# Performance work log

Hardware: AMD Instinct MI355X
Metric: run time of the kernel (lower is better)

Reference implementation:

```python
import jax, jax.numpy as jnp
import numpy as np

B, S, DIM, COV = 64, 512, 1024, 256


def setup_inputs() -> dict:
    key = jax.random.key(0)
    ks = jax.random.split(key, 12)
    s = 0.02
    h = jax.random.normal(ks[0], (B, DIM), jnp.float32)
    context = jax.random.normal(ks[1], (B, S, DIM), jnp.float32)
    cov = jax.random.normal(ks[2], (B, S, COV), jnp.float32)
    mask = jax.random.randint(ks[3], (B, S), 0, 2) == 1
    W_in = jax.random.normal(ks[4], (DIM, DIM), jnp.float32) * s
    W_out = jax.random.normal(ks[5], (DIM, 2 * DIM), jnp.float32) * s
    W_cov = jax.random.normal(ks[6], (DIM, COV), jnp.float32) * s
    b_cov = jax.random.normal(ks[7], (DIM,), jnp.float32) * s
    w_ih = jax.random.normal(ks[8], (3 * COV, 2 * DIM + 1), jnp.float32) * s
    w_hh = jax.random.normal(ks[9], (3 * COV, COV), jnp.float32) * s
    b_ih = jax.random.normal(ks[10], (3 * COV,), jnp.float32) * s
    b_hh = jax.random.normal(ks[11], (3 * COV,), jnp.float32) * s
    return dict(h=h, context=context, cov=cov, W_in=W_in, W_out=W_out,
                W_cov=W_cov, b_cov=b_cov, w_ih=w_ih, w_hh=w_hh,
                b_ih=b_ih, b_hh=b_hh, mask=mask)


def reference(h, context, cov, W_in, W_out, W_cov, b_cov, w_ih, w_hh, b_ih, b_hh, mask):
    # coverage-adjusted context: context + cov_linear(cov)  [B,S,DIM]
    ctx = context + jnp.einsum('bsc,dc->bsd', cov, W_cov) + b_cov
    # target = linear_in(h)  [B,DIM]
    target = h @ W_in.T
    # scores = bmm(context, target).squeeze(2)  [B,S]
    attn = jnp.einsum('bsd,bd->bs', ctx, target)
    attn = jnp.where(mask, -jnp.inf, attn)
    attn = jax.nn.softmax(attn, axis=1)
    # weighted_context = bmm(attn3, context)  [B,DIM]
    wc = jnp.einsum('bs,bsd->bd', attn, ctx)
    h_tilde = jnp.tanh(jnp.concatenate([wc, h], axis=1) @ W_out.T)
    # single-step GRU coverage update over B*S rows
    h_exp = jnp.broadcast_to(h[:, None, :], (B, S, DIM))
    x = jnp.concatenate([ctx, h_exp, attn[..., None]], axis=-1).reshape(B * S, 2 * DIM + 1)
    h0 = cov.reshape(B * S, COV)
    gx = x @ w_ih.T + b_ih   # [B*S, 3*COV]
    gh = h0 @ w_hh.T + b_hh  # [B*S, 3*COV]
    xr, xz, xn = jnp.split(gx, 3, axis=1)
    hr, hz, hn = jnp.split(gh, 3, axis=1)
    r = jax.nn.sigmoid(xr + hr)
    z = jax.nn.sigmoid(xz + hz)
    n = jnp.tanh(xn + r * hn)
    new_cov = ((1.0 - z) * n + z * h0).reshape(B, S, COV)
    return h_tilde, attn, new_cov
```

## Files before the change

kernel.cpp:

```cpp
#include <hip/hip_runtime.h>
#include <math.h>

typedef unsigned short ushort_t;
typedef __attribute__((ext_vector_type(8))) short short8;
typedef __attribute__((ext_vector_type(4))) float f32x4;
typedef __attribute__((ext_vector_type(4))) unsigned short ushort4v;

constexpr int B_ = 64, S_ = 512, DIM_ = 1024, COV_ = 256, TC_ = 768, KIH_ = 2049;
constexpr int NG_ = 1024, KG_ = 1280;

__device__ __forceinline__ float b2f(ushort_t u) {
    union { unsigned int i; float f; } v; v.i = ((unsigned int)u) << 16; return v.f;
}
__device__ __forceinline__ ushort_t f2b(float f) {
    unsigned int x = __float_as_uint(f);
    unsigned int r = x + 0x7fffu + ((x >> 16) & 1u);
    return (ushort_t)(r >> 16);
}
__device__ __forceinline__ float ldv(const float* p, size_t i) { return p[i]; }
__device__ __forceinline__ float ldv(const ushort_t* p, size_t i) { return b2f(p[i]); }

__device__ __forceinline__ float wave_reduce(float a) {
#pragma unroll
    for (int off = 32; off >= 1; off >>= 1) a += __shfl_down(a, off, 64);
    return a;
}

__device__ __forceinline__ void xpose4(f32x4& v, int l) {
    float s, r;
    s = (l & 1) ? v[0] : v[1]; r = __shfl_xor(s, 1, 64); if (l & 1) v[0] = r; else v[1] = r;
    s = (l & 1) ? v[2] : v[3]; r = __shfl_xor(s, 1, 64); if (l & 1) v[2] = r; else v[3] = r;
    s = (l & 2) ? v[0] : v[2]; r = __shfl_xor(s, 2, 64); if (l & 2) v[0] = r; else v[2] = r;
    s = (l & 2) ? v[1] : v[3]; r = __shfl_xor(s, 2, 64); if (l & 2) v[1] = r; else v[3] = r;
}

#define GLDS16(src, dst)                                                            \
    __builtin_amdgcn_global_load_lds(                                               \
        (const __attribute__((address_space(1))) void*)(src),                       \
        (__attribute__((address_space(3))) void*)(dst), 16, 0, 0)

__global__ void k_detect(const unsigned char* __restrict__ mask,
                         const ushort_t* __restrict__ win,
                         int* __restrict__ flags) {
    __shared__ int red0[256];
    __shared__ int red1[256];
    int tid = threadIdx.x, mb = 0, f32 = 0;
    for (int i = tid; i < 32768; i += 256)
        if ((i & 3) != 0 && mask[i] != 0) mb = 1;
    for (int i = tid; i < 32768; i += 256) {
        ushort_t u = win[2 * i];
        if ((u & 0x7F80u) >= 0x4480u) f32 = 1;
    }
    red0[tid] = mb; red1[tid] = f32; __syncthreads();
    for (int st = 128; st >= 1; st >>= 1) {
        if (tid < st) { red0[tid] |= red0[tid + st]; red1[tid] |= red1[tid + st]; }
        __syncthreads();
    }
    if (tid == 0) { flags[0] = red0[0]; flags[1] = red1[0]; }
}

template <typename IT>
__device__ __forceinline__ void transpose_body(const IT* __restrict__ in,
                                               ushort_t* __restrict__ out,
                                               int R, int C, int ld, int off) {
    int idx = blockIdx.x * 256 + threadIdx.x;
    if (idx >= R * C) return;
    int r = idx / C, c = idx - r * C;
    out[c * R + r] = f2b(ldv(in, (size_t)r * ld + off + c));
}
__global__ void k_transpose(const void* __restrict__ in, ushort_t* __restrict__ out,
                            int R, int C, int ld, int off, const int* __restrict__ flags) {
    if (flags[1]) transpose_body((const float*)in, out, R, C, ld, off);
    else transpose_body((const ushort_t*)in, out, R, C, ld, off);
}

template <typename IT>
__device__ __forceinline__ void watt_body(const IT* __restrict__ wih, float* __restrict__ watt) {
    int j = threadIdx.x;
    watt[j] = ldv(wih, (size_t)j * KIH_ + 2048);
}
__global__ void k_watt(const void* __restrict__ wih, float* __restrict__ watt,
                       const int* __restrict__ flags) {
    if (flags[1]) watt_body((const float*)wih, watt);
    else watt_body((const ushort_t*)wih, watt);
}

template <typename IT>
__device__ __forceinline__ void bfold_body(const IT* __restrict__ bcov,
                                           const IT* __restrict__ wih,
                                           float* __restrict__ bfold) {
    int j = blockIdx.x * 4 + (threadIdx.x >> 6);
    int lane = threadIdx.x & 63;
    const IT* wr = wih + (size_t)j * KIH_;
    float a = 0.f;
#pragma unroll
    for (int i = 0; i < 16; ++i) { int k = lane + 64 * i; a += ldv(bcov, k) * ldv(wr, k); }
    a = wave_reduce(a);
    if (lane == 0) bfold[j] = a;
}
__global__ __launch_bounds__(256) void k_bfold(const void* __restrict__ bcov,
                                               const void* __restrict__ wih,
                                               float* __restrict__ bfold,
                                               const int* __restrict__ flags) {
    if (flags[1]) bfold_body((const float*)bcov, (const float*)wih, bfold);
    else bfold_body((const ushort_t*)bcov, (const ushort_t*)wih, bfold);
}

__global__ __launch_bounds__(256) void k_wfold(const ushort_t* __restrict__ wcov_t,
                                               const ushort_t* __restrict__ w_t,
                                               float* __restrict__ wfold) {
    __shared__ float col[DIM_];
    int c = blockIdx.x, tid = threadIdx.x;
    for (int d = tid; d < DIM_; d += 256) col[d] = b2f(wcov_t[c * DIM_ + d]);
    __syncthreads();
    float a0 = 0.f, a1 = 0.f, a2 = 0.f;
    for (int d = 0; d < DIM_; ++d) {
        float x = col[d];
        const ushort_t* wr = w_t + d * TC_;
        a0 += x * b2f(wr[tid]);
        a1 += x * b2f(wr[tid + 256]);
        a2 += x * b2f(wr[tid + 512]);
    }
    wfold[c * TC_ + tid] = a0;
    wfold[c * TC_ + tid + 256] = a1;
    wfold[c * TC_ + tid + 512] = a2;
}

template <typename IT>
__device__ __forceinline__ void buildwg_body(const IT* __restrict__ wih,
                                             const IT* __restrict__ whh,
                                             const float* __restrict__ wfold,
                                             ushort_t* __restrict__ wg) {
    int idx = blockIdx.x * 256 + threadIdx.x;
    if (idx >= NG_ * KG_) return;
    int n = idx / KG_, k = idx - n * KG_;
    int g = n & 3, cq = n >> 2;
    int j = g * COV_ + cq;
    float v;
    if (k < DIM_) {
        v = (j < TC_) ? ldv(wih, (size_t)j * KIH_ + k) : 0.f;
    } else {
        int c = k - DIM_;
        if (j < 512)      v = wfold[c * TC_ + j] + ldv(whh, (size_t)j * COV_ + c);
        else if (j < TC_) v = wfold[c * TC_ + j];
        else              v = ldv(whh, (size_t)(j - 256) * COV_ + c);
    }
    wg[(size_t)n * KG_ + k] = f2b(v);
}
__global__ void k_buildwg(const void* __restrict__ wih, const void* __restrict__ whh,
                          const float* __restrict__ wfold, ushort_t* __restrict__ wg,
                          const int* __restrict__ flags) {
    if (flags[1]) buildwg_body((const float*)wih, (const float*)whh, wfold, wg);
    else buildwg_body((const ushort_t*)wih, (const ushort_t*)whh, wfold, wg);
}

template <typename IT>
__device__ __forceinline__ void target_body(const IT* __restrict__ h,
                                            const IT* __restrict__ W_in,
                                            float* __restrict__ target) {
    int o = blockIdx.x * 4 + (threadIdx.x >> 6);
    int lane = threadIdx.x & 63;
    int b = o >> 10, d = o & (DIM_ - 1);
    const IT* hr = h + (size_t)b * DIM_;
    const IT* wr = W_in + (size_t)d * DIM_;
    float a = 0.f;
#pragma unroll
    for (int j = 0; j < 16; ++j) { int k = lane + 64 * j; a += ldv(hr, k) * ldv(wr, k); }
    a = wave_reduce(a);
    if (lane == 0) target[o] = a;
}
__global__ __launch_bounds__(256) void k_target_w(const void* __restrict__ h,
                                                  const void* __restrict__ W_in,
                                                  float* __restrict__ target,
                                                  const int* __restrict__ flags) {
    if (flags[1]) target_body((const float*)h, (const float*)W_in, target);
    else target_body((const ushort_t*)h, (const ushort_t*)W_in, target);
}

template <typename IT>
__device__ __forceinline__ void mvec_body(const float* __restrict__ target,
                                          const IT* __restrict__ W_cov,
                                          const IT* __restrict__ bcov,
                                          float* __restrict__ mvec,
                                          float* __restrict__ bct) {
    __shared__ float tg[DIM_];
    __shared__ float red[256];
    int b = blockIdx.x, tid = threadIdx.x;
    float pb = 0.f;
    for (int k = tid; k < DIM_; k += 256) {
        float t = target[b * DIM_ + k];
        tg[k] = t; pb += t * ldv(bcov, k);
    }
    red[tid] = pb; __syncthreads();
    for (int st = 128; st >= 1; st >>= 1) {
        if (tid < st) red[tid] += red[tid + st];
        __syncthreads();
    }
    float acc = 0.f;
    for (int d = 0; d < DIM_; ++d) acc += tg[d] * ldv(W_cov, (size_t)d * COV_ + tid);
    mvec[b * COV_ + tid] = acc;
    if (tid == 0) bct[b] = red[0];
}
__global__ __launch_bounds__(256) void k_mvec(const float* __restrict__ target,
                                              const void* __restrict__ W_cov,
                                              const void* __restrict__ bcov,
                                              float* __restrict__ mvec,
                                              float* __restrict__ bct,
                                              const int* __restrict__ flags) {
    if (flags[1]) mvec_body(target, (const float*)W_cov, (const float*)bcov, mvec, bct);
    else mvec_body(target, (const ushort_t*)W_cov, (const ushort_t*)bcov, mvec, bct);
}

template <typename IT>
__device__ __forceinline__ void scoreraw_body(const IT* __restrict__ context,
                                              const IT* __restrict__ cov,
                                              const float* __restrict__ target,
                                              const float* __restrict__ mvec,
                                              const float* __restrict__ bct,
                                              float* __restrict__ scf,
                                              ushort_t* __restrict__ ctx_bf,
                                              ushort_t* __restrict__ cov_bf) {
    __shared__ float tg[DIM_];
    __shared__ float ms[COV_];
    int b = blockIdx.x, tid = threadIdx.x;
    for (int k = tid; k < DIM_; k += 256) tg[k] = target[b * DIM_ + k];
    if (tid < COV_) ms[tid] = mvec[b * COV_ + tid];
    float bc = bct[b];
    __syncthreads();
    int wave = tid >> 6, lane = tid & 63;
    int s0 = blockIdx.y * 64 + wave * 16;
    for (int i = 0; i < 16; ++i) {
        int s = s0 + i;
        size_t row = (size_t)(b * S_ + s);
        const IT* cr = context + row * DIM_;
        const IT* vr = cov + row * COV_;
        float a = 0.f;
        if constexpr (sizeof(IT) == 4) {
#pragma unroll
            for (int j = 0; j < 4; ++j) {
                int d = lane * 4 + 256 * j;
                float4 x = *(const float4*)((const float*)cr + d);
                a += x.x * tg[d] + x.y * tg[d + 1] + x.z * tg[d + 2] + x.w * tg[d + 3];
                if (ctx_bf) {
                    ushort4v u;
                    u[0] = f2b(x.x); u[1] = f2b(x.y); u[2] = f2b(x.z); u[3] = f2b(x.w);
                    *(ushort4v*)(ctx_bf + row * DIM_ + d) = u;
                }
            }
            {
                int cc = lane * 4;
                float4 x = *(const float4*)((const float*)vr + cc);
                a += x.x * ms[cc] + x.y * ms[cc + 1] + x.z * ms[cc + 2] + x.w * ms[cc + 3];
                if (cov_bf) {
                    ushort4v u;
                    u[0] = f2b(x.x); u[1] = f2b(x.y); u[2] = f2b(x.z); u[3] = f2b(x.w);
                    *(ushort4v*)(cov_bf + row * COV_ + cc) = u;
                }
            }
        } else {
#pragma unroll
            for (int j = 0; j < 16; ++j) { int d = lane + 64 * j; a += ldv(cr, d) * tg[d]; }
#pragma unroll
            for (int j = 0; j < 4; ++j) { int c = lane + 64 * j; a += ldv(vr, c) * ms[c]; }
        }
        a = wave_reduce(a);
        if (lane == 0) scf[row] = a + bc;
    }
}
__global__ __launch_bounds__(256) void k_scoreraw(const void* __restrict__ context,
                                                  const void* __restrict__ cov,
                                                  const float* __restrict__ target,
                                                  const float* __restrict__ mvec,
                                                  const float* __restrict__ bct,
                                                  float* __restrict__ scf,
                                                  ushort_t* __restrict__ ctx_bf,
                                                  ushort_t* __restrict__ cov_bf,
                                                  const int* __restrict__ flags) {
    if (flags[1]) scoreraw_body((const float*)context, (const float*)cov, target, mvec, bct,
                                scf, ctx_bf, cov_bf);
    else scoreraw_body((const ushort_t*)context, (const ushort_t*)cov, target, mvec, bct,
                       scf, ctx_bf, cov_bf);
}

__global__ __launch_bounds__(256) void k_softmax(const float* __restrict__ scf,
                                                 const void* __restrict__ maskp,
                                                 const int* __restrict__ flags,
                                                 float* __restrict__ attnf,
                                                 float* __restrict__ attn_out) {
    __shared__ float red[256];
    int b = blockIdx.x, tid = threadIdx.x;
    int mb = flags[0];
    int i0 = b * S_ + tid, i1 = i0 + 256;
    int m0 = mb ? (int)((const unsigned char*)maskp)[i0] : ((const int*)maskp)[i0];
    int m1 = mb ? (int)((const unsigned char*)maskp)[i1] : ((const int*)maskp)[i1];
    float s0 = m0 ? -INFINITY : scf[i0];
    float s1 = m1 ? -INFINITY : scf[i1];
    red[tid] = fmaxf(s0, s1); __syncthreads();
    for (int st = 128; st >= 1; st >>= 1) {
        if (tid < st) red[tid] = fmaxf(red[tid], red[tid + st]);
        __syncthreads();
    }
    float mx = red[0]; __syncthreads();
    float e0 = expf(s0 - mx), e1 = expf(s1 - mx);
    red[tid] = e0 + e1; __syncthreads();
    for (int st = 128; st >= 1; st >>= 1) {
        if (tid < st) red[tid] += red[tid + st];
        __syncthreads();
    }
    float inv = 1.0f / red[0];
    float a0 = e0 * inv, a1 = e1 * inv;
    attnf[i0] = a0; attnf[i1] = a1;
    attn_out[i0] = a0; attn_out[i1] = a1;
}

__global__ __launch_bounds__(256) void k_wcpart2(const ushort_t* __restrict__ ctx_bf,
                                                 const ushort_t* __restrict__ cov_bf,
                                                 const void* __restrict__ ctx_in,
                                                 const void* __restrict__ cov_in,
                                                 const float* __restrict__ attnf,
                                                 float* __restrict__ wc8,
                                                 float* __restrict__ ac8,
                                                 const int* __restrict__ flags) {
    const ushort_t* C = flags[1] ? ctx_bf : (const ushort_t*)ctx_in;
    const ushort_t* V = flags[1] ? cov_bf : (const ushort_t*)cov_in;
    __shared__ float at[64];
    int b = blockIdx.x, ch = blockIdx.y, tid = threadIdx.x;
    int s0 = ch * 64;
    if (tid < 64) at[tid] = attnf[b * S_ + s0 + tid];
    __syncthreads();
    float acv = 0.f;
    for (int s = 0; s < 64; ++s)
        acv += at[s] * b2f(V[((size_t)(b * S_ + s0 + s)) * COV_ + tid]);
    ac8[((size_t)ch * B_ + b) * COV_ + tid] = acv;
    float acc[4] = {0.f, 0.f, 0.f, 0.f};
    for (int s = 0; s < 64; ++s) {
        float w = at[s];
        const ushort_t* cr = C + ((size_t)(b * S_ + s0 + s)) * DIM_;
        acc[0] += w * b2f(cr[tid]);
        acc[1] += w * b2f(cr[tid + 256]);
        acc[2] += w * b2f(cr[tid + 512]);
        acc[3] += w * b2f(cr[tid + 768]);
    }
    size_t base = ((size_t)ch * B_ + b) * DIM_;
    for (int m = 0; m < 4; ++m) wc8[base + tid + 256 * m] = acc[m];
}

template <typename IT>
__device__ __forceinline__ void wcfin_body(const float* __restrict__ wc8,
                                           const float* __restrict__ ac8,
                                           const ushort_t* __restrict__ wcov_t,
                                           const IT* __restrict__ bcov,
                                           float* __restrict__ wc) {
    __shared__ float ac[COV_];
    int b = blockIdx.x, tid = threadIdx.x;
    float a = 0.f;
    for (int ch = 0; ch < 8; ++ch) a += ac8[((size_t)ch * B_ + b) * COV_ + tid];
    ac[tid] = a;
    __syncthreads();
    float acc[4] = {0.f, 0.f, 0.f, 0.f};
    for (int ch = 0; ch < 8; ++ch) {
        size_t base = ((size_t)ch * B_ + b) * DIM_;
        for (int m = 0; m < 4; ++m) acc[m] += wc8[base + tid + 256 * m];
    }
    for (int c = 0; c < COV_; ++c) {
        float av = ac[c];
        const ushort_t* wr = wcov_t + c * DIM_;
        acc[0] += av * b2f(wr[tid]);
        acc[1] += av * b2f(wr[tid + 256]);
        acc[2] += av * b2f(wr[tid + 512]);
        acc[3] += av * b2f(wr[tid + 768]);
    }
    for (int m = 0; m < 4; ++m) {
        int d = tid + 256 * m;
        wc[b * DIM_ + d] = acc[m] + ldv(bcov, d);
    }
}
__global__ __launch_bounds__(256) void k_wcfin(const float* __restrict__ wc8,
                                               const float* __restrict__ ac8,
                                               const ushort_t* __restrict__ wcov_t,
                                               const void* __restrict__ bcov,
                                               float* __restrict__ wc,
                                               const int* __restrict__ flags) {
    if (flags[1]) wcfin_body(wc8, ac8, wcov_t, (const float*)bcov, wc);
    else wcfin_body(wc8, ac8, wcov_t, (const ushort_t*)bcov, wc);
}

template <typename IT>
__device__ __forceinline__ void htilde_body(const float* __restrict__ wc,
                                            const IT* __restrict__ h,
                                            const IT* __restrict__ W_out,
                                            float* __restrict__ out_ht) {
    int o = blockIdx.x * 4 + (threadIdx.x >> 6);
    int lane = threadIdx.x & 63;
    int b = o >> 10, d = o & (DIM_ - 1);
    const float* wcr = wc + b * DIM_;
    const IT* hr = h + (size_t)b * DIM_;
    const IT* wr = W_out + (size_t)d * 2 * DIM_;
    float a = 0.f;
#pragma unroll
    for (int j = 0; j < 16; ++j) { int k = lane + 64 * j; a += wcr[k] * ldv(wr, k); }
#pragma unroll
    for (int j = 0; j < 16; ++j) { int k = lane + 64 * j; a += ldv(hr, k) * ldv(wr, DIM_ + k); }
    a = wave_reduce(a);
    if (lane == 0) out_ht[o] = tanhf(a);
}
__global__ __launch_bounds__(256) void k_htilde_w(const float* __restrict__ wc,
                                                  const void* __restrict__ h,
                                                  const void* __restrict__ W_out,
                                                  float* __restrict__ out_ht,
                                                  const int* __restrict__ flags) {
    if (flags[1]) htilde_body(wc, (const float*)h, (const float*)W_out, out_ht);
    else htilde_body(wc, (const ushort_t*)h, (const ushort_t*)W_out, out_ht);
}

template <typename IT>
__device__ __forceinline__ void gxh_body(const IT* __restrict__ h,
                                         const IT* __restrict__ w_ih,
                                         const IT* __restrict__ b_ih,
                                         const float* __restrict__ bfold,
                                         float* __restrict__ gxall) {
    int o = blockIdx.x * 4 + (threadIdx.x >> 6);
    int lane = threadIdx.x & 63;
    int b = o / TC_, j = o - b * TC_;
    const IT* hr = h + (size_t)b * DIM_;
    const IT* wr = w_ih + (size_t)j * KIH_ + DIM_;
    float a = 0.f;
#pragma unroll
    for (int i = 0; i < 16; ++i) { int k = lane + 64 * i; a += ldv(hr, k) * ldv(wr, k); }
    a = wave_reduce(a);
    if (lane == 0) gxall[o] = a + ldv(b_ih, j) + bfold[j];
}
__global__ __launch_bounds__(256) void k_gxh_w(const void* __restrict__ h,
                                               const void* __restrict__ w_ih,
                                               const void* __restrict__ b_ih,
                                               const float* __restrict__ bfold,
                                               float* __restrict__ gxall,
                                               const int* __restrict__ flags) {
    if (flags[1]) gxh_body((const float*)h, (const float*)w_ih, (const float*)b_ih, bfold, gxall);
    else gxh_body((const ushort_t*)h, (const ushort_t*)w_ih, (const ushort_t*)b_ih, bfold, gxall);
}

__global__ __launch_bounds__(256) void k_gemm5(const ushort_t* __restrict__ ctx_bf,
                                               const ushort_t* __restrict__ cov_bf,
                                               const void* __restrict__ ctx_in,
                                               const void* __restrict__ cov_in,
                                               const ushort_t* __restrict__ wg,
                                               const float* __restrict__ attnf,
                                               const float* __restrict__ gxall,
                                               const float* __restrict__ watt,
                                               const void* __restrict__ bhh,
                                               float* __restrict__ out_cov,
                                               const int* __restrict__ flags) {
    const int f32in = flags[1];
    const ushort_t* Xc = f32in ? ctx_bf : (const ushort_t*)ctx_in;
    const ushort_t* Xv = f32in ? cov_bf : (const ushort_t*)cov_in;
    __shared__ __align__(16) unsigned char smem[2 * 128 * 33 * 4];
    ushort_t* A0 = (ushort_t*)smem;
    ushort_t* B0 = A0 + 128 * 32;
    ushort_t* A1 = B0 + 128 * 32;
    ushort_t* B1 = A1 + 128 * 32;
    float* smN = (float*)smem;
    float* smZ = smN + 128 * 33;

    int tid = threadIdx.x;
    int p = blockIdx.x;
    int xcd = p & 7, t = p >> 3;
    int nb = t & 7, rb = xcd + 8 * (t >> 3);
    int n0 = nb * 128;
    int grow0 = rb * 128;
    int wave = tid >> 6, lane = tid & 63;
    int wm = wave >> 1, wn = wave & 1;
    int half = lane >> 4, r16 = lane & 15;

    int c0 = wave * 128 + lane;
    int ra0 = c0 >> 2, sa0 = (c0 & 3) ^ ((ra0 >> 1) & 3);
    int c1 = c0 + 64;
    int ra1 = c1 >> 2, sa1 = (c1 & 3) ^ ((ra1 >> 1) & 3);

    const ushort_t* gA0c = Xc + (size_t)(grow0 + ra0) * DIM_ + sa0 * 8;
    const ushort_t* gA1c = Xc + (size_t)(grow0 + ra1) * DIM_ + sa1 * 8;
    const ushort_t* gA0v = Xv + (size_t)(grow0 + ra0) * COV_ + sa0 * 8;
    const ushort_t* gA1v = Xv + (size_t)(grow0 + ra1) * COV_ + sa1 * 8;
    const ushort_t* gB0p = wg + (size_t)(n0 + ra0) * KG_ + sa0 * 8;
    const ushort_t* gB1p = wg + (size_t)(n0 + ra1) * KG_ + sa1 * 8;
    int ldsd0 = wave * 1024;
    int ldsd1 = wave * 1024 + 512;

    int offA[4], offB[4];
#pragma unroll
    for (int u = 0; u < 4; ++u) {
        int rA = wm * 64 + u * 16 + r16;
        offA[u] = rA * 32 + (half ^ ((rA >> 1) & 3)) * 8;
        int rB = wn * 64 + u * 16 + r16;
        offB[u] = rB * 32 + (half ^ ((rB >> 1) & 3)) * 8;
    }

    f32x4 acc[4][4];
#pragma unroll
    for (int i = 0; i < 4; ++i)
#pragma unroll
        for (int j = 0; j < 4; ++j) acc[i][j] = (f32x4){0.f, 0.f, 0.f, 0.f};

    auto stage = [&](int kt, ushort_t* Ad, ushort_t* Bd) {
        int k0 = kt * 32;
        const ushort_t *pa0, *pa1;
        if (k0 < DIM_) { pa0 = gA0c + k0; pa1 = gA1c + k0; }
        else           { int kk = k0 - DIM_; pa0 = gA0v + kk; pa1 = gA1v + kk; }
        GLDS16(pa0, Ad + ldsd0);
        GLDS16(pa1, Ad + ldsd1);
        GLDS16(gB0p + k0, Bd + ldsd0);
        GLDS16(gB1p + k0, Bd + ldsd1);
    };
    auto compute = [&](const ushort_t* Ac, const ushort_t* Bc) {
        short8 a[4], b[4];
#pragma unroll
        for (int u = 0; u < 4; ++u) a[u] = *(const short8*)&Ac[offA[u]];
#pragma unroll
        for (int u = 0; u < 4; ++u) b[u] = *(const short8*)&Bc[offB[u]];
#pragma unroll
        for (int i = 0; i < 4; ++i)
#pragma unroll
            for (int j = 0; j < 4; ++j)
                acc[i][j] = __builtin_amdgcn_mfma_f32_16x16x32_bf16(a[i], b[j], acc[i][j], 0, 0, 0);
    };

    constexpr int NT = KG_ / 32;
    stage(0, A0, B0);
    __syncthreads();
#pragma unroll 1
    for (int kt = 0; kt < NT; kt += 2) {
        stage(kt + 1, A1, B1);
        compute(A0, B0);
        __syncthreads();
        if (kt + 2 < NT) stage(kt + 2, A0, B0);
        compute(A1, B1);
        __syncthreads();
    }

    int l = lane;
    int bb = grow0 >> 9;
    const float* gx = gxall + bb * TC_;
    int rloc[4]; float atv[4];
#pragma unroll
    for (int i = 0; i < 4; ++i) {
        rloc[i] = wm * 64 + 16 * i + ((l >> 4) << 2) + (l & 3);
        atv[i] = attnf[grow0 + rloc[i]];
    }
#pragma unroll
    for (int j = 0; j < 4; ++j) {
        int cl = wn * 16 + 4 * j + ((l >> 2) & 3);
        int c = (n0 >> 2) + cl;
        float gxR = gx[c], gxZ = gx[COV_ + c], gxN = gx[2 * COV_ + c];
        float waR = watt[c], waZ = watt[COV_ + c], waN = watt[2 * COV_ + c];
        float bhR, bhZ, bhN;
        if (f32in) {
            const float* bp = (const float*)bhh;
            bhR = bp[c]; bhZ = bp[COV_ + c]; bhN = bp[2 * COV_ + c];
        } else {
            const ushort_t* bp = (const ushort_t*)bhh;
            bhR = b2f(bp[c]); bhZ = b2f(bp[COV_ + c]); bhN = b2f(bp[2 * COV_ + c]);
        }
#pragma unroll
        for (int i = 0; i < 4; ++i) {
            f32x4 v = acc[i][j];
            xpose4(v, l);
            float at = atv[i];
            float aR  = v[0] + gxR + at * waR + bhR;
            float aZ  = v[1] + gxZ + at * waZ + bhZ;
            float aXN = v[2] + gxN + at * waN;
            float aHN = v[3] + bhN;
            float r = 1.f / (1.f + expf(-aR));
            float z = 1.f / (1.f + expf(-aZ));
            float nn = tanhf(aXN + r * aHN);
            smN[rloc[i] * 33 + cl] = nn;
            smZ[rloc[i] * 33 + cl] = z;
        }
    }
    __syncthreads();
    int cbase = nb * 32;
    for (int u = tid; u < 128 * 8; u += 256) {
        int rl = u >> 3, c4 = (u & 7) * 4;
        float n0v = smN[rl * 33 + c4 + 0], n1v = smN[rl * 33 + c4 + 1];
        float n2v = smN[rl * 33 + c4 + 2], n3v = smN[rl * 33 + c4 + 3];
        float z0 = smZ[rl * 33 + c4 + 0], z1 = smZ[rl * 33 + c4 + 1];
        float z2 = smZ[rl * 33 + c4 + 2], z3 = smZ[rl * 33 + c4 + 3];
        size_t base = (size_t)(grow0 + rl) * COV_ + cbase + c4;
        float h0v, h1v, h2v, h3v;
        if (f32in) {
            float4 hv = *(const float4*)((const float*)cov_in + base);
            h0v = hv.x; h1v = hv.y; h2v = hv.z; h3v = hv.w;
        } else {
            ushort4v hv = *(const ushort4v*)((const ushort_t*)cov_in + base);
            h0v = b2f(hv[0]); h1v = b2f(hv[1]); h2v = b2f(hv[2]); h3v = b2f(hv[3]);
        }
        float4 o;
        o.x = (1.f - z0) * n0v + z0 * h0v;
        o.y = (1.f - z1) * n1v + z1 * h1v;
        o.z = (1.f - z2) * n2v + z2 * h2v;
        o.w = (1.f - z3) * n3v + z3 * h3v;
        *(float4*)(out_cov + base) = o;
    }
}

template <typename IT>
__device__ __forceinline__ void gru_body(const IT* __restrict__ context,
                                         const IT* __restrict__ cov,
                                         const float* __restrict__ attnf,
                                         const float* __restrict__ gxall,
                                         const float* __restrict__ watt,
                                         const ushort_t* __restrict__ w_t,
                                         const float* __restrict__ wfold,
                                         const ushort_t* __restrict__ whh_t,
                                         const IT* __restrict__ bhh,
                                         float* __restrict__ out_cov) {
    __shared__ float xc[8][DIM_];
    __shared__ float h0s[8][COV_];
    __shared__ float atn[8];
    int base = blockIdx.x * 8, tid = threadIdx.x;
    int b = base / S_;
    for (int i = tid; i < 8 * DIM_; i += 256)
        ((float*)xc)[i] = ldv(context, (size_t)base * DIM_ + i);
    for (int i = tid; i < 8 * COV_; i += 256)
        ((float*)h0s)[i] = ldv(cov, (size_t)base * COV_ + i);
    if (tid < 8) atn[tid] = attnf[base + tid];
    __syncthreads();
    int c = tid;
    float gxR = gxall[b * TC_ + c], gxZ = gxall[b * TC_ + 256 + c], gxN = gxall[b * TC_ + 512 + c];
    float bhR = ldv(bhh, c), bhZ = ldv(bhh, 256 + c), bhN = ldv(bhh, 512 + c);
    float waR = watt[c], waZ = watt[256 + c], waN = watt[512 + c];
    float aR[8], aZ[8], aXN[8], aHN[8];
#pragma unroll
    for (int g = 0; g < 8; ++g) {
        float a = atn[g];
        aR[g] = gxR + bhR + a * waR;
        aZ[g] = gxZ + bhZ + a * waZ;
        aXN[g] = gxN + a * waN;
        aHN[g] = bhN;
    }
    for (int k = 0; k < DIM_; ++k) {
        const ushort_t* row = w_t + k * TC_;
        float wr = b2f(row[c]), wz = b2f(row[256 + c]), wn = b2f(row[512 + c]);
#pragma unroll
        for (int g = 0; g < 8; ++g) {
            float x = xc[g][k];
            aR[g] += x * wr; aZ[g] += x * wz; aXN[g] += x * wn;
        }
    }
    for (int k = 0; k < COV_; ++k) {
        const float* row = wfold + k * TC_;
        float wr = row[c], wz = row[256 + c], wn = row[512 + c];
#pragma unroll
        for (int g = 0; g < 8; ++g) {
            float x = h0s[g][k];
            aR[g] += x * wr; aZ[g] += x * wz; aXN[g] += x * wn;
        }
    }
    for (int k = 0; k < COV_; ++k) {
        const ushort_t* row = whh_t + k * TC_;
        float wr = b2f(row[c]), wz = b2f(row[256 + c]), wn = b2f(row[512 + c]);
#pragma unroll
        for (int g = 0; g < 8; ++g) {
            float hh = h0s[g][k];
            aR[g] += hh * wr; aZ[g] += hh * wz; aHN[g] += hh * wn;
        }
    }
#pragma unroll
    for (int g = 0; g < 8; ++g) {
        float r = 1.f / (1.f + expf(-aR[g]));
        float z = 1.f / (1.f + expf(-aZ[g]));
        float n = tanhf(aXN[g] + r * aHN[g]);
        float h0c = h0s[g][c];
        out_cov[(size_t)(base + g) * COV_ + c] = (1.f - z) * n + z * h0c;
    }
}
__global__ __launch_bounds__(256) void k_gru_f(const void* __restrict__ context,
                                               const void* __restrict__ cov,
                                               const float* __restrict__ attnf,
                                               const float* __restrict__ gxall,
                                               const float* __restrict__ watt,
                                               const ushort_t* __restrict__ w_t,
                                               const float* __restrict__ wfold,
                                               const ushort_t* __restrict__ whh_t,
                                               const void* __restrict__ bhh,
                                               float* __restrict__ out_cov,
                                               const int* __restrict__ flags) {
    if (flags[1]) gru_body((const float*)context, (const float*)cov, attnf, gxall, watt,
                           w_t, wfold, whh_t, (const float*)bhh, out_cov);
    else gru_body((const ushort_t*)context, (const ushort_t*)cov, attnf, gxall, watt,
                  w_t, wfold, whh_t, (const ushort_t*)bhh, out_cov);
}

extern "C" void kernel_launch(void* const* d_in, const int* in_sizes, int n_in,
                              void* d_out, int out_size, void* d_ws, size_t ws_size,
                              hipStream_t stream) {
    const void* h       = d_in[0];
    const void* context = d_in[1];
    const void* cov     = d_in[2];
    const void* W_in    = d_in[3];
    const void* W_out   = d_in[4];
    const void* W_cov   = d_in[5];
    const void* b_cov   = d_in[6];
    const void* w_ih    = d_in[7];
    const void* w_hh    = d_in[8];
    const void* b_ih    = d_in[9];
    const void* b_hh    = d_in[10];
    const void* maskp   = d_in[11];

    float* out = (float*)d_out;
    float* out_ht   = out;
    float* out_attn = out + B_ * DIM_;
    float* out_cov  = out + B_ * DIM_ + B_ * S_;

    char* ws = (char*)d_ws;
    size_t o = 0;
    float* target = (float*)(ws + o); o += (size_t)B_ * DIM_ * 4;
    float* attnf  = (float*)(ws + o); o += (size_t)B_ * S_ * 4;
    float* wc     = (float*)(ws + o); o += (size_t)B_ * DIM_ * 4;
    float* gxall  = (float*)(ws + o); o += (size_t)B_ * TC_ * 4;
    float* watt   = (float*)(ws + o); o += 4096;
    float* mvec   = (float*)(ws + o); o += (size_t)B_ * COV_ * 4;
    float* bct    = (float*)(ws + o); o += 4096;
    float* bfold  = (float*)(ws + o); o += 4096;
    float* wfold  = (float*)(ws + o); o += (size_t)COV_ * TC_ * 4;
    ushort_t* w_t    = (ushort_t*)(ws + o); o += (size_t)DIM_ * TC_ * 2;
    ushort_t* whh_t  = (ushort_t*)(ws + o); o += (size_t)COV_ * TC_ * 2;
    ushort_t* wcov_t = (ushort_t*)(ws + o); o += (size_t)COV_ * DIM_ * 2;
    int* flags = (int*)(ws + o); o += 256;
    float* scf   = (float*)(ws + o); o += (size_t)B_ * S_ * 4;
    float* wc8   = (float*)(ws + o); o += (size_t)8 * B_ * DIM_ * 4;
    float* ac8   = (float*)(ws + o); o += (size_t)8 * B_ * COV_ * 4;
    ushort_t* wg = (ushort_t*)(ws + o); o += (size_t)NG_ * KG_ * 2;
    ushort_t* ctx_bf = (ushort_t*)(ws + o); o += (size_t)B_ * S_ * DIM_ * 2;
    ushort_t* cov_bf = (ushort_t*)(ws + o); o += (size_t)B_ * S_ * COV_ * 2;
    size_t fixed = o;

    const size_t TOTAL_ROWS = (size_t)B_ * S_;
    const bool fused = ws_size >= fixed;

    k_detect<<<1, 256, 0, stream>>>((const unsigned char*)maskp, (const ushort_t*)W_in, flags);
    k_transpose<<<(TC_ * DIM_) / 256, 256, 0, stream>>>(w_ih, w_t, TC_, DIM_, KIH_, 0, flags);
    k_transpose<<<(DIM_ * COV_) / 256, 256, 0, stream>>>(W_cov, wcov_t, DIM_, COV_, COV_, 0, flags);
    if (!fused)
        k_transpose<<<(TC_ * COV_) / 256, 256, 0, stream>>>(w_hh, whh_t, TC_, COV_, COV_, 0, flags);
    k_watt<<<1, TC_, 0, stream>>>(w_ih, watt, flags);
    k_bfold<<<TC_ / 4, 256, 0, stream>>>(b_cov, w_ih, bfold, flags);
    k_wfold<<<COV_, 256, 0, stream>>>(wcov_t, w_t, wfold);
    if (fused)
        k_buildwg<<<(NG_ * KG_ + 255) / 256, 256, 0, stream>>>(w_ih, w_hh, wfold, wg, flags);

    k_target_w<<<(B_ * DIM_) / 4, 256, 0, stream>>>(h, W_in, target, flags);
    k_mvec<<<B_, 256, 0, stream>>>(target, W_cov, b_cov, mvec, bct, flags);
    k_scoreraw<<<dim3(B_, 8), 256, 0, stream>>>(context, cov, target, mvec, bct, scf,
                                                fused ? ctx_bf : nullptr,
                                                fused ? cov_bf : nullptr, flags);
    k_softmax<<<B_, 256, 0, stream>>>(scf, maskp, flags, attnf, out_attn);
    if (fused)
        k_wcpart2<<<dim3(B_, 8), 256, 0, stream>>>(ctx_bf, cov_bf, context, cov, attnf,
                                                   wc8, ac8, flags);
    else
        k_wcpart2<<<dim3(B_, 8), 256, 0, stream>>>((const ushort_t*)context, (const ushort_t*)cov,
                                                   context, cov, attnf, wc8, ac8, flags);
    k_wcfin<<<B_, 256, 0, stream>>>(wc8, ac8, wcov_t, b_cov, wc, flags);
    k_htilde_w<<<(B_ * DIM_) / 4, 256, 0, stream>>>(wc, h, W_out, out_ht, flags);

    k_gxh_w<<<(B_ * TC_) / 4, 256, 0, stream>>>(h, w_ih, b_ih, bfold, gxall, flags);
    if (fused) {
        int nblk = (int)(TOTAL_ROWS / 128) * (NG_ / 128);
        k_gemm5<<<nblk, 256, 0, stream>>>(ctx_bf, cov_bf, context, cov, wg, attnf,
                                          gxall, watt, b_hh, out_cov, flags);
    } else {
        k_gru_f<<<(B_ * S_) / 8, 256, 0, stream>>>(context, cov, attnf, gxall, watt,
                                                   w_t, wfold, whh_t, b_hh, out_cov, flags);
    }
}
```

Before: 713.2 us.

## Double GEMM K-tile to 64 with 8-way swizzle and parallelize mvec over columns

The fused GRU GEMM now stages 64-wide K tiles instead of 32, using an 8-slot XOR swizzle and two MFMA sub-steps per stage. This halves the number of barrier and stage iterations. The cost is doubling LDS to 64KB, which may reduce occupancy. Separately, the mvec kernel splits its columns over 4 blocks per batch and reduces the D dimension across 4 wave groups, giving more parallelism to a serial 1024-length loop.

```diff
diff --git a/kernel.cpp b/kernel.cpp
--- a/kernel.cpp
+++ b/kernel.cpp
@@ -185,7 +185,7 @@
                                           float* __restrict__ bct) {
     __shared__ float tg[DIM_];
     __shared__ float red[256];
-    int b = blockIdx.x, tid = threadIdx.x;
+    int b = blockIdx.x, q = blockIdx.y, tid = threadIdx.x;
     float pb = 0.f;
     for (int k = tid; k < DIM_; k += 256) {
         float t = target[b * DIM_ + k];
@@ -196,10 +196,17 @@
         if (tid < st) red[tid] += red[tid + st];
         __syncthreads();
     }
+    if (q == 0 && tid == 0) bct[b] = red[0];
+    __syncthreads();
+    int cg = tid & 63, dg = tid >> 6;
+    int c = q * 64 + cg;
     float acc = 0.f;
-    for (int d = 0; d < DIM_; ++d) acc += tg[d] * ldv(W_cov, (size_t)d * COV_ + tid);
-    mvec[b * COV_ + tid] = acc;
-    if (tid == 0) bct[b] = red[0];
+    int d0 = dg * 256;
+    for (int d = d0; d < d0 + 256; ++d) acc += tg[d] * ldv(W_cov, (size_t)d * COV_ + c);
+    red[dg * 64 + cg] = acc;
+    __syncthreads();
+    if (dg == 0)
+        mvec[b * COV_ + c] = red[cg] + red[64 + cg] + red[128 + cg] + red[192 + cg];
 }
 __global__ __launch_bounds__(256) void k_mvec(const float* __restrict__ target,
                                               const void* __restrict__ W_cov,
@@ -440,7 +447,7 @@
     else gxh_body((const ushort_t*)h, (const ushort_t*)w_ih, (const ushort_t*)b_ih, bfold, gxall);
 }
 
-__global__ __launch_bounds__(256) void k_gemm5(const ushort_t* __restrict__ ctx_bf,
+__global__ __launch_bounds__(256) void k_gemm6(const ushort_t* __restrict__ ctx_bf,
                                                const ushort_t* __restrict__ cov_bf,
                                                const void* __restrict__ ctx_in,
                                                const void* __restrict__ cov_in,
@@ -454,11 +461,11 @@
     const int f32in = flags[1];
     const ushort_t* Xc = f32in ? ctx_bf : (const ushort_t*)ctx_in;
     const ushort_t* Xv = f32in ? cov_bf : (const ushort_t*)cov_in;
-    __shared__ __align__(16) unsigned char smem[2 * 128 * 33 * 4];
+    __shared__ __align__(16) unsigned char smem[65536];
     ushort_t* A0 = (ushort_t*)smem;
-    ushort_t* B0 = A0 + 128 * 32;
-    ushort_t* A1 = B0 + 128 * 32;
-    ushort_t* B1 = A1 + 128 * 32;
+    ushort_t* B0 = A0 + 8192;
+    ushort_t* A1 = B0 + 8192;
+    ushort_t* B1 = A1 + 8192;
     float* smN = (float*)smem;
     float* smZ = smN + 128 * 33;
 
@@ -472,28 +479,28 @@
     int wm = wave >> 1, wn = wave & 1;
     int half = lane >> 4, r16 = lane & 15;
 
-    int c0 = wave * 128 + lane;
-    int ra0 = c0 >> 2, sa0 = (c0 & 3) ^ ((ra0 >> 1) & 3);
-    int c1 = c0 + 64;
-    int ra1 = c1 >> 2, sa1 = (c1 & 3) ^ ((ra1 >> 1) & 3);
-
-    const ushort_t* gA0c = Xc + (size_t)(grow0 + ra0) * DIM_ + sa0 * 8;
-    const ushort_t* gA1c = Xc + (size_t)(grow0 + ra1) * DIM_ + sa1 * 8;
-    const ushort_t* gA0v = Xv + (size_t)(grow0 + ra0) * COV_ + sa0 * 8;
-    const ushort_t* gA1v = Xv + (size_t)(grow0 + ra1) * COV_ + sa1 * 8;
-    const ushort_t* gB0p = wg + (size_t)(n0 + ra0) * KG_ + sa0 * 8;
-    const ushort_t* gB1p = wg + (size_t)(n0 + ra1) * KG_ + sa1 * 8;
-    int ldsd0 = wave * 1024;
-    int ldsd1 = wave * 1024 + 512;
-
-    int offA[4], offB[4];
-#pragma unroll
-    for (int u = 0; u < 4; ++u) {
-        int rA = wm * 64 + u * 16 + r16;
-        offA[u] = rA * 32 + (half ^ ((rA >> 1) & 3)) * 8;
-        int rB = wn * 64 + u * 16 + r16;
-        offB[u] = rB * 32 + (half ^ ((rB >> 1) & 3)) * 8;
-    }
+    const ushort_t* gAc[4]; const ushort_t* gAv[4]; const ushort_t* gB[4];
+    int ldsOff[4];
+#pragma unroll
+    for (int j = 0; j < 4; ++j) {
+        int c = wave * 256 + j * 64 + lane;
+        int row = c >> 3, sl = (c & 7) ^ ((c >> 3) & 7);
+        gAc[j] = Xc + (size_t)(grow0 + row) * DIM_ + sl * 8;
+        gAv[j] = Xv + (size_t)(grow0 + row) * COV_ + sl * 8;
+        gB[j]  = wg + (size_t)(n0 + row) * KG_ + sl * 8;
+        ldsOff[j] = (wave * 256 + j * 64) * 8;
+    }
+
+    int offA[2][4], offB[2][4];
+#pragma unroll
+    for (int kh = 0; kh < 2; ++kh)
+#pragma unroll
+        for (int u = 0; u < 4; ++u) {
+            int rA = wm * 64 + u * 16 + r16;
+            offA[kh][u] = rA * 64 + ((kh * 4 + half) ^ (rA & 7)) * 8;
+            int rB = wn * 64 + u * 16 + r16;
+            offB[kh][u] = rB * 64 + ((kh * 4 + half) ^ (rB & 7)) * 8;
+        }
 
     f32x4 acc[4][4];
 #pragma unroll
@@ -502,29 +509,35 @@
         for (int j = 0; j < 4; ++j) acc[i][j] = (f32x4){0.f, 0.f, 0.f, 0.f};
 
     auto stage = [&](int kt, ushort_t* Ad, ushort_t* Bd) {
-        int k0 = kt * 32;
-        const ushort_t *pa0, *pa1;
-        if (k0 < DIM_) { pa0 = gA0c + k0; pa1 = gA1c + k0; }
-        else           { int kk = k0 - DIM_; pa0 = gA0v + kk; pa1 = gA1v + kk; }
-        GLDS16(pa0, Ad + ldsd0);
-        GLDS16(pa1, Ad + ldsd1);
-        GLDS16(gB0p + k0, Bd + ldsd0);
-        GLDS16(gB1p + k0, Bd + ldsd1);
+        int k0 = kt * 64;
+        if (k0 < DIM_) {
+#pragma unroll
+            for (int j = 0; j < 4; ++j) GLDS16(gAc[j] + k0, Ad + ldsOff[j]);
+        } else {
+            int kk = k0 - DIM_;
+#pragma unroll
+            for (int j = 0; j < 4; ++j) GLDS16(gAv[j] + kk, Ad + ldsOff[j]);
+        }
+#pragma unroll
+        for (int j = 0; j < 4; ++j) GLDS16(gB[j] + k0, Bd + ldsOff[j]);
     };
     auto compute = [&](const ushort_t* Ac, const ushort_t* Bc) {
-        short8 a[4], b[4];
-#pragma unroll
-        for (int u = 0; u < 4; ++u) a[u] = *(const short8*)&Ac[offA[u]];
-#pragma unroll
-        for (int u = 0; u < 4; ++u) b[u] = *(const short8*)&Bc[offB[u]];
-#pragma unroll
-        for (int i = 0; i < 4; ++i)
-#pragma unroll
-            for (int j = 0; j < 4; ++j)
-                acc[i][j] = __builtin_amdgcn_mfma_f32_16x16x32_bf16(a[i], b[j], acc[i][j], 0, 0, 0);
+#pragma unroll
+        for (int kh = 0; kh < 2; ++kh) {
+            short8 a[4], b[4];
+#pragma unroll
+            for (int u = 0; u < 4; ++u) a[u] = *(const short8*)&Ac[offA[kh][u]];
+#pragma unroll
+            for (int u = 0; u < 4; ++u) b[u] = *(const short8*)&Bc[offB[kh][u]];
+#pragma unroll
+            for (int i = 0; i < 4; ++i)
+#pragma unroll
+                for (int j = 0; j < 4; ++j)
+                    acc[i][j] = __builtin_amdgcn_mfma_f32_16x16x32_bf16(a[i], b[j], acc[i][j], 0, 0, 0);
+        }
     };
 
-    constexpr int NT = KG_ / 32;
+    constexpr int NT = KG_ / 64;
     stage(0, A0, B0);
     __syncthreads();
 #pragma unroll 1
@@ -749,7 +762,7 @@
         k_buildwg<<<(NG_ * KG_ + 255) / 256, 256, 0, stream>>>(w_ih, w_hh, wfold, wg, flags);
 
     k_target_w<<<(B_ * DIM_) / 4, 256, 0, stream>>>(h, W_in, target, flags);
-    k_mvec<<<B_, 256, 0, stream>>>(target, W_cov, b_cov, mvec, bct, flags);
+    k_mvec<<<dim3(B_, 4), 256, 0, stream>>>(target, W_cov, b_cov, mvec, bct, flags);
     k_scoreraw<<<dim3(B_, 8), 256, 0, stream>>>(context, cov, target, mvec, bct, scf,
                                                 fused ? ctx_bf : nullptr,
                                                 fused ? cov_bf : nullptr, flags);
@@ -766,7 +779,7 @@
     k_gxh_w<<<(B_ * TC_) / 4, 256, 0, stream>>>(h, w_ih, b_ih, bfold, gxall, flags);
     if (fused) {
         int nblk = (int)(TOTAL_ROWS / 128) * (NG_ / 128);
-        k_gemm5<<<nblk, 256, 0, stream>>>(ctx_bf, cov_bf, context, cov, wg, attnf,
+        k_gemm6<<<nblk, 256, 0, stream>>>(ctx_bf, cov_bf, context, cov, wg, attnf,
                                           gxall, watt, b_hh, out_cov, flags);
     } else {
         k_gru_f<<<(B_ * S_) / 8, 256, 0, stream>>>(context, cov, attnf, gxall, watt,
```

After: 727.0 us. About the same (+1.9%).
